# Optimization experiments

Hardware: AMD Instinct MI355X
Metric: run time of the kernel (lower is better)

## Reference

```python
import jax, jax.numpy as jnp
import numpy as np

H, D = 8, 32
IN, HID, OUT = 256, 256, 128
N_PAR, N_FIG, N_TAB, N_CIT = 100000, 20000, 20000, 50000
E = 200000


def setup_inputs() -> dict:
    key = jax.random.key(0)
    ks = iter(jax.random.split(key, 80))
    def nrm(shape, s=0.05):
        return jax.random.normal(next(ks), shape, dtype=jnp.float32) * s
    def ridx(n):
        return jax.random.randint(next(ks), (E,), 0, n, dtype=jnp.int32)
    inp = {
        'x_par': nrm((N_PAR, IN), 1.0), 'x_fig': nrm((N_FIG, IN), 1.0),
        'x_tab': nrm((N_TAB, IN), 1.0), 'x_cit': nrm((N_CIT, IN), 1.0),
    }
    for t in ['par', 'fig', 'tab', 'cit']:
        inp[f'Wp_{t}'] = nrm((IN, HID)); inp[f'bp_{t}'] = nrm((HID,))
    for et in ['pf', 'fp', 'pt', 'tp', 'pc', 'cp']:
        inp[f'a_{et}_s'] = nrm((H, D)); inp[f'a_{et}_d'] = nrm((H, D))
    inp['k_w'] = nrm((HID, HID)); inp['k_b'] = nrm((HID,)); inp['q'] = nrm((HID,))
    for t in ['par', 'fig', 'tab', 'cit']:
        inp[f'Wh_{t}'] = nrm((HID, OUT)); inp[f'bh_{t}'] = nrm((OUT,))
    inp['cls_w'] = nrm((2 * OUT, 1)); inp['cls_b'] = nrm((1,))
    inp['pf_src'] = ridx(N_PAR); inp['pf_dst'] = ridx(N_FIG)
    inp['fp_src'] = ridx(N_FIG); inp['fp_dst'] = ridx(N_PAR)
    inp['pt_src'] = ridx(N_PAR); inp['pt_dst'] = ridx(N_TAB)
    inp['tp_src'] = ridx(N_TAB); inp['tp_dst'] = ridx(N_PAR)
    inp['pc_src'] = ridx(N_PAR); inp['pc_dst'] = ridx(N_CIT)
    inp['cp_src'] = ridx(N_CIT); inp['cp_dst'] = ridx(N_PAR)
    inp['target_node_idx'] = 5
    return inp


def _agg(xs, xd, si, di, a_s, a_d, n_dst):
    # HANConv metapath aggregation: GAT-style attention + per-dst softmax + scatter-sum + relu
    as_ = jnp.einsum('nhd,hd->nh', xs, a_s)            # [Ns,H]
    ad_ = jnp.einsum('nhd,hd->nh', xd, a_d)            # [Nd,H]
    alpha = jax.nn.leaky_relu(as_[si] + ad_[di], 0.2)  # [E,H]
    m = jax.ops.segment_max(alpha, di, num_segments=n_dst)
    m = jnp.where(jnp.isfinite(m), m, 0.0)
    ex = jnp.exp(alpha - m[di])
    den = jax.ops.segment_sum(ex, di, num_segments=n_dst)
    w = ex / (den[di] + 1e-16)
    out = jax.ops.segment_sum(xs[si] * w[:, :, None], di, num_segments=n_dst)  # [Nd,H,D]
    return jax.nn.relu(out.reshape(n_dst, H * D))


def _group(outs, q, kw, kb):
    # HANConv semantic (metapath-level) attention
    st = jnp.stack(outs)                               # [M,N,F]
    kmean = jnp.tanh(st @ kw + kb).mean(axis=1)        # [M,F]
    attn = jax.nn.softmax(kmean @ q)                   # [M]
    return jnp.einsum('m,mnf->nf', attn, st)


def reference(x_par, x_fig, x_tab, x_cit,
              Wp_par, bp_par, Wp_fig, bp_fig, Wp_tab, bp_tab, Wp_cit, bp_cit,
              a_pf_s, a_pf_d, a_fp_s, a_fp_d, a_pt_s, a_pt_d,
              a_tp_s, a_tp_d, a_pc_s, a_pc_d, a_cp_s, a_cp_d,
              k_w, k_b, q,
              Wh_par, bh_par, Wh_fig, bh_fig, Wh_tab, bh_tab, Wh_cit, bh_cit,
              cls_w, cls_b,
              pf_src, pf_dst, fp_src, fp_dst, pt_src, pt_dst,
              tp_src, tp_dst, pc_src, pc_dst, cp_src, cp_dst,
              target_node_idx):
    # per-node-type input projection
    h_par = (x_par @ Wp_par + bp_par).reshape(-1, H, D)
    h_fig = (x_fig @ Wp_fig + bp_fig).reshape(-1, H, D)
    h_tab = (x_tab @ Wp_tab + bp_tab).reshape(-1, H, D)
    h_cit = (x_cit @ Wp_cit + bp_cit).reshape(-1, H, D)
    # per-metapath message passing, grouped per destination node type
    o_fig = _group([_agg(h_par, h_fig, pf_src, pf_dst, a_pf_s, a_pf_d, N_FIG)], q, k_w, k_b)
    o_tab = _group([_agg(h_par, h_tab, pt_src, pt_dst, a_pt_s, a_pt_d, N_TAB)], q, k_w, k_b)
    o_cit = _group([_agg(h_par, h_cit, pc_src, pc_dst, a_pc_s, a_pc_d, N_CIT)], q, k_w, k_b)
    o_par = _group([
        _agg(h_fig, h_par, fp_src, fp_dst, a_fp_s, a_fp_d, N_PAR),
        _agg(h_tab, h_par, tp_src, tp_dst, a_tp_s, a_tp_d, N_PAR),
        _agg(h_cit, h_par, cp_src, cp_dst, a_cp_s, a_cp_d, N_PAR),
    ], q, k_w, k_b)
    # output heads (table/cited_paper heads computed in the original but unused for scores)
    par_emb = o_par @ Wh_par + bh_par
    fig_emb = o_fig @ Wh_fig + bh_fig
    _ = o_tab @ Wh_tab + bh_tab
    _ = o_cit @ Wh_cit + bh_cit
    # pairwise classifier: target figure embedding broadcast against every paragraph
    target = fig_emb[target_node_idx]
    comb = jnp.concatenate(
        [jnp.broadcast_to(target[None, :], (par_emb.shape[0], OUT)), par_emb], axis=1)
    scores = (comb @ cls_w + cls_b)[:, 0]
    return scores
```

## Files before the change

kernel.cpp:

```cpp
#include <hip/hip_runtime.h>
#include <hip/hip_bf16.h>
#include <math.h>

typedef float f32x4 __attribute__((ext_vector_type(4)));
typedef short bf16x8 __attribute__((ext_vector_type(8)));

#define NPAR 100000
#define NFIG 20000
#define NTAB 20000
#define NCIT 50000
#define NEDGE 200000
#define CAP 32
#define PFCAP 79

__device__ __forceinline__ unsigned short f2b(float f) {
    union { float f; unsigned u; } x; x.f = f;
    unsigned r = x.u + 0x7FFFu + ((x.u >> 16) & 1u);
    return (unsigned short)(r >> 16);
}
__device__ __forceinline__ float b2f(unsigned short b) {
    union { unsigned u; float f; } x; x.u = ((unsigned)b) << 16; return x.f;
}
__device__ __forceinline__ float fast_tanh(float x) {
    float e = __expf(2.f * x);
    return 1.f - 2.f * __builtin_amdgcn_rcpf(e + 1.f);
}
__device__ __forceinline__ void async_copy16(const unsigned short* g, unsigned short* l) {
    __builtin_amdgcn_global_load_lds(
        (const __attribute__((address_space(1))) unsigned int*)g,
        (__attribute__((address_space(3))) unsigned int*)l, 16, 0, 0);
}

__global__ void k_transpose5(const float* __restrict__ W0, const float* __restrict__ W1,
                             const float* __restrict__ W2, const float* __restrict__ W3,
                             const float* __restrict__ W4, unsigned short* __restrict__ WT) {
    int b = blockIdx.x, which = b >> 8, k = b & 255, n = threadIdx.x;
    const float* W = which == 0 ? W0 : which == 1 ? W1 : which == 2 ? W2 : which == 3 ? W3 : W4;
    WT[(size_t)which * 65536 + n * 256 + k] = f2b(W[k * 256 + n]);
}

__global__ void k_precompute(const float* __restrict__ WhF, const float* __restrict__ bhF,
                             const float* __restrict__ WhP, const float* __restrict__ bhP,
                             const float* __restrict__ clsw, const float* __restrict__ clsb,
                             float* __restrict__ u, float* __restrict__ v, float* __restrict__ smallb) {
    int t = threadIdx.x;
    float su = 0.f, sv = 0.f;
    for (int j = 0; j < 128; ++j) {
        su += WhF[t * 128 + j] * clsw[j];
        sv += WhP[t * 128 + j] * clsw[128 + j];
    }
    u[t] = su; v[t] = sv;
    if (t == 0) {
        float c = clsb[0];
        for (int j = 0; j < 128; ++j) c += bhF[j] * clsw[j] + bhP[j] * clsw[128 + j];
        smallb[264] = c;
    }
}

__global__ void k_edges(const int* __restrict__ d0, const int* __restrict__ d1,
                        const int* __restrict__ d2, int* __restrict__ count,
                        int* __restrict__ elist,
                        const int* __restrict__ psrc, const int* __restrict__ pdst,
                        const int* __restrict__ tgtp, int* __restrict__ mlist) {
    int b = blockIdx.x;
    int m = b / 782;
    int e = (b - m * 782) * 256 + threadIdx.x;
    if (e >= NEDGE) return;
    if (m < 3) {
        const int* dst = m == 0 ? d0 : m == 1 ? d1 : d2;
        int d = dst[e];
        int* cnt = count + (size_t)m * NPAR;
        int* el = elist + (size_t)m * NPAR * CAP;
        int slot = atomicAdd(&cnt[d], 1);
        if (slot < CAP) el[(size_t)d * CAP + slot] = e;
    } else {
        if (pdst[e] == tgtp[0]) {
            int slot = atomicAdd(&mlist[0], 1);
            if (slot < PFCAP) mlist[1 + slot] = psrc[e];
        }
    }
}

struct ProjPack {
    const float* X[4];
    const unsigned short* WT[4];
    const float* bias[4];
    unsigned short* H[4];
    const float* av[16];
    float* ov[16];
    int nrows[4];
    int bbase[4];
    int nv[4];
};

#define LOADA(k0, A0, A1) do { \
    const float4* _p = reinterpret_cast<const float4*>(Arow + (k0)); \
    A0 = _p[0]; A1 = _p[1]; } while (0)
#define WRITEA(buf, A0, A1) do { \
    __align__(16) unsigned short _t[8]; \
    _t[0] = f2b(A0.x); _t[1] = f2b(A0.y); _t[2] = f2b(A0.z); _t[3] = f2b(A0.w); \
    _t[4] = f2b(A1.x); _t[5] = f2b(A1.y); _t[6] = f2b(A1.z); _t[7] = f2b(A1.w); \
    *reinterpret_cast<uint4*>(&As[buf][arow * 32 + acol]) = *reinterpret_cast<const uint4*>(_t); } while (0)

__global__ __launch_bounds__(512, 4) void k_gemm_proj(ProjPack p) {
    __shared__ __align__(16) unsigned short As[2][128 * 32];
    __shared__ __align__(16) unsigned short Bs[2][256 * 32];
    int bid = blockIdx.x;
    int ty = (bid >= p.bbase[1]) + (bid >= p.bbase[2]) + (bid >= p.bbase[3]);
    int m0 = (bid - p.bbase[ty]) * 128;
    const float* Xf = p.X[ty];
    const unsigned short* B = p.WT[ty];
    unsigned short* Hout = p.H[ty];
    int Nrows = p.nrows[ty];
    int nv = p.nv[ty];

    int t = threadIdx.x, l = t & 63, w = t >> 6;
    int wm = (w >> 2) * 64, wn = (w & 3) * 64;
    int lr = l & 15, hi = l >> 4;
    int arow = t >> 2, acol = (t & 3) * 8;
    int arow_c = m0 + arow; if (arow_c > Nrows - 1) arow_c = Nrows - 1;
    const float* Arow = Xf + (size_t)arow_c * 256 + acol;
    f32x4 acc[4][4] = {};
    float4 aP0, aP1, aQ0, aQ1;

    auto stageB = [&](int buf, int k0) {
#pragma unroll
        for (int i = 0; i < 2; ++i) {
            int rowb = w * 32 + i * 16;
            async_copy16(B + (size_t)(rowb + (l >> 2)) * 256 + k0 + (l & 3) * 8,
                         &Bs[buf][rowb * 32]);
        }
    };

    LOADA(0, aP0, aP1);
    stageB(0, 0);
    WRITEA(0, aP0, aP1);
    LOADA(32, aQ0, aQ1);
    asm volatile("s_waitcnt vmcnt(2) lgkmcnt(0)" ::: "memory");
    __builtin_amdgcn_s_barrier();

#pragma unroll
    for (int ks = 0; ks < 8; ++ks) {
        int cur = ks & 1;
        if (ks < 7) stageB(cur ^ 1, (ks + 1) * 32);
        if (ks < 6) {
            if ((ks & 1) == 0) LOADA((ks + 2) * 32, aP0, aP1);
            else               LOADA((ks + 2) * 32, aQ0, aQ1);
        }
        bf16x8 af[4], bfr[4];
#pragma unroll
        for (int mm = 0; mm < 4; ++mm)
            af[mm] = *reinterpret_cast<const bf16x8*>(&As[cur][(wm + mm * 16 + lr) * 32 + hi * 8]);
#pragma unroll
        for (int nn = 0; nn < 4; ++nn)
            bfr[nn] = *reinterpret_cast<const bf16x8*>(&Bs[cur][(wn + nn * 16 + lr) * 32 + hi * 8]);
#pragma unroll
        for (int mm = 0; mm < 4; ++mm)
#pragma unroll
            for (int nn = 0; nn < 4; ++nn)
                acc[mm][nn] = __builtin_amdgcn_mfma_f32_16x16x32_bf16(bfr[nn], af[mm], acc[mm][nn], 0, 0, 0);
        if (ks < 7) {
            if ((ks & 1) == 0) WRITEA(cur ^ 1, aQ0, aQ1);
            else               WRITEA(cur ^ 1, aP0, aP1);
            if (ks < 6) asm volatile("s_waitcnt vmcnt(2) lgkmcnt(0)" ::: "memory");
            else        asm volatile("s_waitcnt vmcnt(0) lgkmcnt(0)" ::: "memory");
            __builtin_amdgcn_s_barrier();
        }
    }

    __syncthreads();
    float* sattp = (float*)&As[0][0];
    unsigned short* Hst = &Bs[0][0];

    float4 bv4[4], av4[4][4];
#pragma unroll
    for (int nn = 0; nn < 4; ++nn)
        bv4[nn] = *reinterpret_cast<const float4*>(p.bias[ty] + wn + nn * 16 + hi * 4);
#pragma unroll
    for (int v = 0; v < 4; ++v)
        if (v < nv) {
            const float* A = p.av[ty * 4 + v];
#pragma unroll
            for (int nn = 0; nn < 4; ++nn)
                av4[v][nn] = *reinterpret_cast<const float4*>(A + wn + nn * 16 + hi * 4);
        }
    int h0 = (w & 3) * 2;
#pragma unroll
    for (int mm = 0; mm < 4; ++mm) {
        int lrow = wm + mm * 16 + lr;
        float sv[4][2] = {};
#pragma unroll
        for (int nn = 0; nn < 4; ++nn) {
            float c0 = acc[mm][nn][0] + bv4[nn].x;
            float c1 = acc[mm][nn][1] + bv4[nn].y;
            float c2 = acc[mm][nn][2] + bv4[nn].z;
            float c3 = acc[mm][nn][3] + bv4[nn].w;
#pragma unroll
            for (int v = 0; v < 4; ++v)
                if (v < nv)
                    sv[v][nn >> 1] += c0 * av4[v][nn].x + c1 * av4[v][nn].y +
                                      c2 * av4[v][nn].z + c3 * av4[v][nn].w;
        }
#pragma unroll
        for (int v = 0; v < 4; ++v)
            if (v < nv) {
#pragma unroll
                for (int hp = 0; hp < 2; ++hp) {
                    float s = sv[v][hp];
                    s += __shfl_xor(s, 16); s += __shfl_xor(s, 32);
                    if (hi == 0) sattp[v * 1024 + lrow * 8 + h0 + hp] = s;
                }
            }
    }

    if (ty != 0) {
        for (int hf = 0; hf < 2; ++hf) {
            if ((w >> 2) == hf) {
#pragma unroll
                for (int mm = 0; mm < 4; ++mm) {
                    int lr2 = mm * 16 + lr;
                    int swz = (lr2 & 7) << 4;
#pragma unroll
                    for (int nn = 0; nn < 4; ++nn) {
                        int colb = (wn + nn * 16 + hi * 4) * 2;
                        ushort4 o;
                        o.x = f2b(acc[mm][nn][0] + bv4[nn].x);
                        o.y = f2b(acc[mm][nn][1] + bv4[nn].y);
                        o.z = f2b(acc[mm][nn][2] + bv4[nn].z);
                        o.w = f2b(acc[mm][nn][3] + bv4[nn].w);
                        *reinterpret_cast<ushort4*>((char*)Hst + lr2 * 512 + (colb ^ swz)) = o;
                    }
                }
            }
            __syncthreads();
            {
                int row = t >> 3;
                int g = m0 + hf * 64 + row;
                if (g < Nrows) {
                    int swz = (row & 7) << 4;
#pragma unroll
                    for (int pass = 0; pass < 4; ++pass) {
                        int c = (t & 7) + pass * 8;
                        uint4 val = *reinterpret_cast<const uint4*>(
                            (const char*)Hst + row * 512 + ((c * 16) ^ swz));
                        *reinterpret_cast<uint4*>(Hout + (size_t)g * 256 + c * 8) = val;
                    }
                }
            }
            __syncthreads();
        }
    } else {
        __syncthreads();
    }

    for (int i = t; i < nv * 1024; i += 512) {
        int v = i >> 10, rem = i & 1023, lrow = rem >> 3, hd = rem & 7;
        int g = m0 + lrow;
        if (g < Nrows) p.ov[ty * 4 + v][(size_t)g * 8 + hd] = sattp[v * 1024 + lrow * 8 + hd];
    }
}

__global__ void k_pf_proj(const int* __restrict__ mlist, const float* __restrict__ Xp,
                          const unsigned short* __restrict__ WTp, const float* __restrict__ bp,
                          unsigned short* __restrict__ Hs) {
    int b = blockIdx.x;
    int cnt = mlist[0]; if (cnt > PFCAP) cnt = PFCAP;
    if (b >= cnt) return;
    int s = mlist[1 + b];
    __shared__ float xr[256];
    int t = threadIdx.x;
    xr[t] = Xp[(size_t)s * 256 + t];
    __syncthreads();
    const unsigned short* wrow = WTp + (size_t)t * 256;
    float acc = bp[t];
    for (int k = 0; k < 256; k += 8) {
        uint4 wv = *reinterpret_cast<const uint4*>(wrow + k);
        unsigned wsv[4] = { wv.x, wv.y, wv.z, wv.w };
#pragma unroll
        for (int j = 0; j < 4; ++j) {
            acc += xr[k + j * 2]     * b2f((unsigned short)(wsv[j] & 0xffffu));
            acc += xr[k + j * 2 + 1] * b2f((unsigned short)(wsv[j] >> 16));
        }
    }
    Hs[(size_t)b * 256 + t] = f2b(acc);
}

struct GKPack {
    const int* src[3]; const int* count[3]; const int* elist[3];
    const unsigned short* H[3]; const float* as_[3]; const float* ad_[3];
    const unsigned short* Bw; const float* kb; const float* v;
    float* ksum[3]; float* gout[3];
};
__global__ __launch_bounds__(512, 4) void k_gather_kmean(GKPack p) {
    __shared__ __align__(16) unsigned short Ar[64 * 256];
    __shared__ __align__(16) unsigned short Bs[256 * 32];
    int bid = blockIdx.x;
    int m = bid / 1563, b2 = bid - m * 1563;
    const int* src = p.src[m];
    const int* count = p.count[m];
    const int* elist = p.elist[m];
    const unsigned short* Hsrc = p.H[m];
    const float* as_ = p.as_[m];
    const float* ad_ = p.ad_[m];
    const unsigned short* Bw = p.Bw;
    int t = threadIdx.x, l = t & 63, w = t >> 6;
    int m0 = b2 * 64;
    int lg = l & 15, gb = l & 48;
    float* ks_rep = p.ksum[m] + (size_t)(b2 & 7) * 256;

    auto stageB = [&](int k0) {
#pragma unroll
        for (int i = 0; i < 2; ++i) {
            int rowb = w * 32 + i * 16;
            async_copy16(Bw + (size_t)(rowb + (l >> 2)) * 256 + k0 + (l & 3) * 8,
                         &Bs[rowb * 32]);
        }
    };
    stageB(0);

    int cnt_[2], s1_[2], s2_[2], ld_[2]; float adh_[2]; bool val_[2];
#pragma unroll
    for (int j = 0; j < 2; ++j) {
        int ld = w * 8 + j * 4 + (l >> 4);
        int d = m0 + ld;
        bool valid = d < NPAR;
        int cnt = 0;
        if (valid) { cnt = count[d]; if (cnt > CAP) cnt = CAP; }
        int e1 = (lg < cnt) ? elist[(size_t)d * CAP + lg] : -1;
        int e2 = (lg + 16 < cnt) ? elist[(size_t)d * CAP + lg + 16] : -1;
        ld_[j] = ld; val_[j] = valid; cnt_[j] = cnt;
        s1_[j] = (e1 >= 0) ? src[e1] : 0;
        s2_[j] = (e2 >= 0) ? src[e2] : 0;
        adh_[j] = valid ? ad_[d * 8 + (lg >> 1)] : 0.f;
    }

    float4 vv0 = *reinterpret_cast<const float4*>(p.v + lg * 16);
    float4 vv1 = *reinterpret_cast<const float4*>(p.v + lg * 16 + 4);
    float4 vv2 = *reinterpret_cast<const float4*>(p.v + lg * 16 + 8);
    float4 vv3 = *reinterpret_cast<const float4*>(p.v + lg * 16 + 12);
    float vr[16] = { vv0.x, vv0.y, vv0.z, vv0.w, vv1.x, vv1.y, vv1.z, vv1.w,
                     vv2.x, vv2.y, vv2.z, vv2.w, vv3.x, vv3.y, vv3.z, vv3.w };

#pragma unroll
    for (int j = 0; j < 2; ++j) {
        int cnt = cnt_[j], s1 = s1_[j], s2 = s2_[j], ld = ld_[j];
        float adh = adh_[j];
        float ar[16];
#pragma unroll
        for (int k = 0; k < 16; ++k) ar[k] = 0.f;
        float den = 0.f;
        int sC = __shfl(s1, gb);
        const uint4* hp0 = reinterpret_cast<const uint4*>(Hsrc + (size_t)sC * 256 + lg * 16);
        uint4 hA = {}, hB = {};
        float asv = 0.f;
        if (cnt > 0) { hA = hp0[0]; hB = hp0[1]; asv = as_[sC * 8 + (lg >> 1)]; }
        for (int i = 0; i < cnt; ++i) {
            int iN = i + 1;
            uint4 nA = {}, nB = {};
            float nas = 0.f;
            if (iN < cnt) {
                int sN = (iN < 16) ? __shfl(s1, gb + (iN & 15)) : __shfl(s2, gb + ((iN - 16) & 15));
                const uint4* np = reinterpret_cast<const uint4*>(Hsrc + (size_t)sN * 256 + lg * 16);
                nA = np[0]; nB = np[1];
                nas = as_[sN * 8 + (lg >> 1)];
            }
            float al = asv + adh;
            al = al > 0.f ? al : 0.2f * al;
            float ex = __expf(al); den += ex;
            unsigned wds[8] = { hA.x, hA.y, hA.z, hA.w, hB.x, hB.y, hB.z, hB.w };
#pragma unroll
            for (int k = 0; k < 8; ++k) {
                ar[k * 2]     += ex * b2f((unsigned short)(wds[k] & 0xffffu));
                ar[k * 2 + 1] += ex * b2f((unsigned short)(wds[k] >> 16));
            }
            hA = nA; hB = nB; asv = nas;
        }
        float inv = 1.f / (den + 1e-16f);
        float gs = 0.f;
        __align__(16) unsigned short ob[16];
#pragma unroll
        for (int k = 0; k < 16; ++k) {
            float r = fmaxf(ar[k] * inv, 0.f);
            gs += r * vr[k];
            ob[k] = f2b(r);
        }
        int u0 = (lg * 2) ^ (ld & 7), u1 = (lg * 2 + 1) ^ (ld & 7);
        *reinterpret_cast<uint4*>(&Ar[ld * 256 + u0 * 8]) = *reinterpret_cast<const uint4*>(ob);
        *reinterpret_cast<uint4*>(&Ar[ld * 256 + u1 * 8]) = *reinterpret_cast<const uint4*>(ob + 8);
        gs += __shfl_xor(gs, 1); gs += __shfl_xor(gs, 2); gs += __shfl_xor(gs, 4); gs += __shfl_xor(gs, 8);
        if (lg == 0 && val_[j]) p.gout[m][m0 + ld] = gs;
    }
    __syncthreads();

    int wm = (w >> 2) * 32, wn = (w & 3) * 64, lr = l & 15, hi = l >> 4;
    f32x4 acc[2][4] = {};
    for (int ks = 0; ks < 8; ++ks) {
        if (ks > 0) {
            __syncthreads();
            stageB(ks * 32);
            __syncthreads();
        }
        bf16x8 af[2], bfr[4];
#pragma unroll
        for (int mm = 0; mm < 2; ++mm) {
            int rr = wm + mm * 16 + lr;
            af[mm] = *reinterpret_cast<const bf16x8*>(&Ar[rr * 256 + (((ks * 4 + hi) ^ (rr & 7)) * 8)]);
        }
#pragma unroll
        for (int nn = 0; nn < 4; ++nn)
            bfr[nn] = *reinterpret_cast<const bf16x8*>(&Bs[(wn + nn * 16 + lr) * 32 + hi * 8]);
#pragma unroll
        for (int mm = 0; mm < 2; ++mm)
#pragma unroll
            for (int nn = 0; nn < 4; ++nn)
                acc[mm][nn] = __builtin_amdgcn_mfma_f32_16x16x32_bf16(af[mm], bfr[nn], acc[mm][nn], 0, 0, 0);
    }
#pragma unroll
    for (int nn = 0; nn < 4; ++nn) {
        int col = wn + nn * 16 + lr;
        float kbv = p.kb[col];
        float cs = 0.f;
#pragma unroll
        for (int mm = 0; mm < 2; ++mm)
#pragma unroll
            for (int r = 0; r < 4; ++r) {
                int row = m0 + wm + mm * 16 + hi * 4 + r;
                if (row < NPAR) cs += fast_tanh(acc[mm][nn][r] + kbv);
            }
        cs += __shfl_xor(cs, 16);
        cs += __shfl_xor(cs, 32);
        if (hi == 0) atomicAdd(&ks_rep[col], cs);
    }
}

__global__ void k_pf_acc(const int* __restrict__ mlist, const int* __restrict__ tgtp,
                         const unsigned short* __restrict__ Hs,
                         const float* __restrict__ as_pf, const float* __restrict__ ad_pf,
                         float* __restrict__ smallb) {
    __shared__ float sacc[4][256];
    __shared__ float sden[4][8];
    int t = threadIdx.x, w = t >> 6, l = t & 63;
    int tgt = tgtp[0];
    int cnt = mlist[0]; if (cnt > PFCAP) cnt = PFCAP;
    int h = l >> 3;
    float adh = ad_pf[tgt * 8 + h];
    float a0 = 0.f, a1 = 0.f, a2 = 0.f, a3 = 0.f, den = 0.f;
    for (int i = w; i < cnt; i += 4) {
        int s = mlist[1 + i];
        float al = as_pf[s * 8 + h] + adh;
        al = al > 0.f ? al : 0.2f * al;
        float ex = __expf(al);
        ushort4 hv = *reinterpret_cast<const ushort4*>(&Hs[(size_t)i * 256 + l * 4]);
        a0 += ex * b2f(hv.x); a1 += ex * b2f(hv.y); a2 += ex * b2f(hv.z); a3 += ex * b2f(hv.w);
        den += ex;
    }
    sacc[w][l * 4 + 0] = a0; sacc[w][l * 4 + 1] = a1;
    sacc[w][l * 4 + 2] = a2; sacc[w][l * 4 + 3] = a3;
    if ((l & 7) == 0) sden[w][h] = den;
    __syncthreads();
    smallb[t] = sacc[0][t] + sacc[1][t] + sacc[2][t] + sacc[3][t];
    if (t < 8) smallb[256 + t] = sden[0][t] + sden[1][t] + sden[2][t] + sden[3][t];
}

__global__ void k_finalize(const float* __restrict__ kacc, const float* __restrict__ q,
                           const float* __restrict__ u, float* __restrict__ smallb) {
    __shared__ float red[256];
    __shared__ float sm[3];
    int t = threadIdx.x;
    float qv = q[t];
    for (int m = 0; m < 3; ++m) {
        float acc = 0.f;
#pragma unroll
        for (int rep = 0; rep < 8; ++rep) acc += kacc[m * 2048 + rep * 256 + t];
        red[t] = acc * qv;
        __syncthreads();
        for (int s = 128; s > 0; s >>= 1) { if (t < s) red[t] += red[t + s]; __syncthreads(); }
        if (t == 0) sm[m] = red[0] / (float)NPAR;
        __syncthreads();
    }
    float den = smallb[256 + (t >> 5)];
    float rt = fmaxf(smallb[t] / (den + 1e-16f), 0.f);
    red[t] = rt * u[t];
    __syncthreads();
    for (int s = 128; s > 0; s >>= 1) { if (t < s) red[t] += red[t + s]; __syncthreads(); }
    if (t == 0) {
        float mx = fmaxf(sm[0], fmaxf(sm[1], sm[2]));
        float e0 = expf(sm[0] - mx), e1 = expf(sm[1] - mx), e2 = expf(sm[2] - mx);
        float sd = e0 + e1 + e2;
        smallb[265] = e0 / sd; smallb[266] = e1 / sd; smallb[267] = e2 / sd;
        smallb[268] = red[0] + smallb[264];
    }
}

__global__ void k_scores(const float* __restrict__ g, const float* __restrict__ smallb,
                         float* __restrict__ out) {
    int i = blockIdx.x * 256 + threadIdx.x;
    if (i >= NPAR) return;
    out[i] = smallb[268] + smallb[265] * g[i] + smallb[266] * g[NPAR + i] + smallb[267] * g[2 * NPAR + i];
}

extern "C" void kernel_launch(void* const* d_in, const int* in_sizes, int n_in,
                              void* d_out, int out_size, void* d_ws, size_t ws_size,
                              hipStream_t stream) {
    char* base = (char*)d_ws;
    size_t off = 0;
    auto alloc = [&](size_t b) -> void* { void* p = base + off; off += (b + 255) & ~(size_t)255; return p; };

    unsigned short* Hsmall = (unsigned short*)alloc((size_t)PFCAP * 256 * 2);
    unsigned short* h_fig = (unsigned short*)alloc((size_t)NFIG * 256 * 2);
    unsigned short* h_tab = (unsigned short*)alloc((size_t)NTAB * 256 * 2);
    unsigned short* h_cit = (unsigned short*)alloc((size_t)NCIT * 256 * 2);
    unsigned short* WTall = (unsigned short*)alloc((size_t)5 * 65536 * 2);
    unsigned short* WT_par = WTall, *WT_fig = WTall + 65536, *WT_tab = WTall + 2 * 65536,
                  *WT_cit = WTall + 3 * 65536, *kwT = WTall + 4 * 65536;
    float* as_pf = (float*)alloc((size_t)NPAR * 8 * 4);
    float* ad_fp = (float*)alloc((size_t)NPAR * 8 * 4);
    float* ad_tp = (float*)alloc((size_t)NPAR * 8 * 4);
    float* ad_cp = (float*)alloc((size_t)NPAR * 8 * 4);
    float* as_fp = (float*)alloc((size_t)NFIG * 8 * 4);
    float* ad_pf = (float*)alloc((size_t)NFIG * 8 * 4);
    float* as_tp = (float*)alloc((size_t)NTAB * 8 * 4);
    float* as_cp = (float*)alloc((size_t)NCIT * 8 * 4);
    float* gbuf  = (float*)alloc((size_t)3 * NPAR * 4);
    int* count3  = (int*)alloc((size_t)3 * NPAR * 4);
    int* elist3  = (int*)alloc((size_t)3 * NPAR * CAP * 4);
    float* kacc  = (float*)alloc((size_t)3 * 8 * 256 * 4);
    float* smallb = (float*)alloc(512 * 4);
    int* mlist   = (int*)alloc((1 + PFCAP) * 4);
    float* uvec  = (float*)alloc(256 * 4);
    float* vvec  = (float*)alloc(256 * 4);

    hipMemsetAsync(kacc, 0, 24576 + 2048 + 512, stream);
    hipMemsetAsync(count3, 0, (size_t)3 * NPAR * 4, stream);

    k_transpose5<<<5 * 256, 256, 0, stream>>>((const float*)d_in[4], (const float*)d_in[6],
                                              (const float*)d_in[8], (const float*)d_in[10],
                                              (const float*)d_in[24], WTall);

    k_precompute<<<1, 256, 0, stream>>>((const float*)d_in[29], (const float*)d_in[30],
                                        (const float*)d_in[27], (const float*)d_in[28],
                                        (const float*)d_in[35], (const float*)d_in[36],
                                        uvec, vvec, smallb);

    k_edges<<<4 * 782, 256, 0, stream>>>((const int*)d_in[40], (const int*)d_in[44],
                                         (const int*)d_in[48], count3, elist3,
                                         (const int*)d_in[37], (const int*)d_in[38],
                                         (const int*)d_in[49], mlist);
    k_pf_proj<<<PFCAP, 256, 0, stream>>>(mlist, (const float*)d_in[0], WT_par,
                                         (const float*)d_in[5], Hsmall);

    ProjPack pp;
    pp.X[0] = (const float*)d_in[0]; pp.X[1] = (const float*)d_in[1];
    pp.X[2] = (const float*)d_in[2]; pp.X[3] = (const float*)d_in[3];
    pp.WT[0] = WT_par; pp.WT[1] = WT_fig; pp.WT[2] = WT_tab; pp.WT[3] = WT_cit;
    pp.bias[0] = (const float*)d_in[5]; pp.bias[1] = (const float*)d_in[7];
    pp.bias[2] = (const float*)d_in[9]; pp.bias[3] = (const float*)d_in[11];
    pp.H[0] = h_fig; pp.H[1] = h_fig; pp.H[2] = h_tab; pp.H[3] = h_cit;
    pp.nrows[0] = NPAR; pp.nrows[1] = NFIG; pp.nrows[2] = NTAB; pp.nrows[3] = NCIT;
    pp.bbase[0] = 0; pp.bbase[1] = 782; pp.bbase[2] = 939; pp.bbase[3] = 1096;
    pp.nv[0] = 4; pp.nv[1] = 2; pp.nv[2] = 1; pp.nv[3] = 1;
    for (int i = 0; i < 16; ++i) { pp.av[i] = nullptr; pp.ov[i] = nullptr; }
    pp.av[0] = (const float*)d_in[12]; pp.ov[0] = as_pf;
    pp.av[1] = (const float*)d_in[15]; pp.ov[1] = ad_fp;
    pp.av[2] = (const float*)d_in[19]; pp.ov[2] = ad_tp;
    pp.av[3] = (const float*)d_in[23]; pp.ov[3] = ad_cp;
    pp.av[4] = (const float*)d_in[14]; pp.ov[4] = as_fp;
    pp.av[5] = (const float*)d_in[13]; pp.ov[5] = ad_pf;
    pp.av[8] = (const float*)d_in[18]; pp.ov[8] = as_tp;
    pp.av[12] = (const float*)d_in[22]; pp.ov[12] = as_cp;
    k_gemm_proj<<<1487, 512, 0, stream>>>(pp);

    k_pf_acc<<<1, 256, 0, stream>>>(mlist, (const int*)d_in[49], Hsmall, as_pf, ad_pf, smallb);

    GKPack gk;
    gk.src[0] = (const int*)d_in[39]; gk.src[1] = (const int*)d_in[43]; gk.src[2] = (const int*)d_in[47];
    gk.count[0] = count3; gk.count[1] = count3 + NPAR; gk.count[2] = count3 + 2 * NPAR;
    gk.elist[0] = elist3; gk.elist[1] = elist3 + (size_t)NPAR * CAP; gk.elist[2] = elist3 + (size_t)2 * NPAR * CAP;
    gk.H[0] = h_fig; gk.H[1] = h_tab; gk.H[2] = h_cit;
    gk.as_[0] = as_fp; gk.as_[1] = as_tp; gk.as_[2] = as_cp;
    gk.ad_[0] = ad_fp; gk.ad_[1] = ad_tp; gk.ad_[2] = ad_cp;
    gk.Bw = kwT; gk.kb = (const float*)d_in[25]; gk.v = vvec;
    gk.ksum[0] = kacc; gk.ksum[1] = kacc + 2048; gk.ksum[2] = kacc + 4096;
    gk.gout[0] = gbuf; gk.gout[1] = gbuf + NPAR; gk.gout[2] = gbuf + 2 * NPAR;
    k_gather_kmean<<<3 * 1563, 512, 0, stream>>>(gk);

    k_finalize<<<1, 256, 0, stream>>>(kacc, (const float*)d_in[26], uvec, smallb);
    k_scores<<<391, 256, 0, stream>>>(gbuf, smallb, (float*)d_out);
}
```

Measured before the change: 355.7 us.

## Batch neighbor gathers four at a time and read GEMM weights directly from global

```diff
diff --git a/kernel.cpp b/kernel.cpp
--- a/kernel.cpp
+++ b/kernel.cpp
@@ -293,7 +293,6 @@
 };
 __global__ __launch_bounds__(512, 4) void k_gather_kmean(GKPack p) {
     __shared__ __align__(16) unsigned short Ar[64 * 256];
-    __shared__ __align__(16) unsigned short Bs[256 * 32];
     int bid = blockIdx.x;
     int m = bid / 1563, b2 = bid - m * 1563;
     const int* src = p.src[m];
@@ -308,16 +307,6 @@
     int lg = l & 15, gb = l & 48;
     float* ks_rep = p.ksum[m] + (size_t)(b2 & 7) * 256;
 
-    auto stageB = [&](int k0) {
-#pragma unroll
-        for (int i = 0; i < 2; ++i) {
-            int rowb = w * 32 + i * 16;
-            async_copy16(Bw + (size_t)(rowb + (l >> 2)) * 256 + k0 + (l & 3) * 8,
-                         &Bs[rowb * 32]);
-        }
-    };
-    stageB(0);
-
     int cnt_[2], s1_[2], s2_[2], ld_[2]; float adh_[2]; bool val_[2];
 #pragma unroll
     for (int j = 0; j < 2; ++j) {
@@ -349,31 +338,37 @@
 #pragma unroll
         for (int k = 0; k < 16; ++k) ar[k] = 0.f;
         float den = 0.f;
-        int sC = __shfl(s1, gb);
-        const uint4* hp0 = reinterpret_cast<const uint4*>(Hsrc + (size_t)sC * 256 + lg * 16);
-        uint4 hA = {}, hB = {};
-        float asv = 0.f;
-        if (cnt > 0) { hA = hp0[0]; hB = hp0[1]; asv = as_[sC * 8 + (lg >> 1)]; }
-        for (int i = 0; i < cnt; ++i) {
-            int iN = i + 1;
-            uint4 nA = {}, nB = {};
-            float nas = 0.f;
-            if (iN < cnt) {
-                int sN = (iN < 16) ? __shfl(s1, gb + (iN & 15)) : __shfl(s2, gb + ((iN - 16) & 15));
-                const uint4* np = reinterpret_cast<const uint4*>(Hsrc + (size_t)sN * 256 + lg * 16);
-                nA = np[0]; nB = np[1];
-                nas = as_[sN * 8 + (lg >> 1)];
+        for (int base = 0; base < cnt; base += 4) {
+            uint4 hA[4], hB[4];
+            float asv[4];
+#pragma unroll
+            for (int b = 0; b < 4; ++b) {
+                int idx = base + b;
+                if (idx < cnt) {
+                    int s = (idx < 16) ? __shfl(s1, gb + (idx & 15)) : __shfl(s2, gb + ((idx - 16) & 15));
+                    const uint4* hp = reinterpret_cast<const uint4*>(Hsrc + (size_t)s * 256 + lg * 16);
+                    hA[b] = hp[0]; hB[b] = hp[1];
+                    asv[b] = as_[s * 8 + (lg >> 1)];
+                } else {
+                    hA[b] = uint4{0, 0, 0, 0}; hB[b] = uint4{0, 0, 0, 0}; asv[b] = 0.f;
+                }
             }
-            float al = asv + adh;
-            al = al > 0.f ? al : 0.2f * al;
-            float ex = __expf(al); den += ex;
-            unsigned wds[8] = { hA.x, hA.y, hA.z, hA.w, hB.x, hB.y, hB.z, hB.w };
-#pragma unroll
-            for (int k = 0; k < 8; ++k) {
-                ar[k * 2]     += ex * b2f((unsigned short)(wds[k] & 0xffffu));
-                ar[k * 2 + 1] += ex * b2f((unsigned short)(wds[k] >> 16));
+#pragma unroll
+            for (int b = 0; b < 4; ++b) {
+                int idx = base + b;
+                if (idx < cnt) {
+                    float al = asv[b] + adh;
+                    al = al > 0.f ? al : 0.2f * al;
+                    float ex = __expf(al); den += ex;
+                    unsigned wds[8] = { hA[b].x, hA[b].y, hA[b].z, hA[b].w,
+                                        hB[b].x, hB[b].y, hB[b].z, hB[b].w };
+#pragma unroll
+                    for (int k = 0; k < 8; ++k) {
+                        ar[k * 2]     += ex * b2f((unsigned short)(wds[k] & 0xffffu));
+                        ar[k * 2 + 1] += ex * b2f((unsigned short)(wds[k] >> 16));
+                    }
+                }
             }
-            hA = nA; hB = nB; asv = nas;
         }
         float inv = 1.f / (den + 1e-16f);
         float gs = 0.f;
@@ -394,21 +389,18 @@
 
     int wm = (w >> 2) * 32, wn = (w & 3) * 64, lr = l & 15, hi = l >> 4;
     f32x4 acc[2][4] = {};
+#pragma unroll
     for (int ks = 0; ks < 8; ++ks) {
-        if (ks > 0) {
-            __syncthreads();
-            stageB(ks * 32);
-            __syncthreads();
-        }
         bf16x8 af[2], bfr[4];
+#pragma unroll
+        for (int nn = 0; nn < 4; ++nn)
+            bfr[nn] = *reinterpret_cast<const bf16x8*>(
+                Bw + (size_t)(wn + nn * 16 + lr) * 256 + ks * 32 + hi * 8);
 #pragma unroll
         for (int mm = 0; mm < 2; ++mm) {
             int rr = wm + mm * 16 + lr;
             af[mm] = *reinterpret_cast<const bf16x8*>(&Ar[rr * 256 + (((ks * 4 + hi) ^ (rr & 7)) * 8)]);
         }
-#pragma unroll
-        for (int nn = 0; nn < 4; ++nn)
-            bfr[nn] = *reinterpret_cast<const bf16x8*>(&Bs[(wn + nn * 16 + lr) * 32 + hi * 8]);
 #pragma unroll
         for (int mm = 0; mm < 2; ++mm)
 #pragma unroll
```

Result: slower. 404.1 us (+13.6%).
